# Kernel tuning notes

Hardware: AMD Instinct MI355X
Metric: run time of the kernel (lower is better)

Reference implementation:

```python
import jax, jax.numpy as jnp
import numpy as np

N_R = 20          # cfg['n_r']
H = 0.01          # cfg['h'] integration step
ALPHA_N = 0.1     # alpha(D_s_n, R_s_n) folded scale (stable: |eig(H*matAn)| << 2.8)
ALPHA_P = 0.08    # alpha(D_s_p, R_s_p)
BETA_N = -0.5     # -beta(...) for negative electrode
BETA_P = 0.4      # beta(...) for positive electrode


def _make_mats():
    n = N_R - 1
    # FDM tridiagonal (1,-2,1) radial diffusion stencil (spm_model.matA)
    matA = (jnp.diag(-2.0 * jnp.ones(n))
            + jnp.diag(jnp.ones(n - 1), 1)
            + jnp.diag(jnp.ones(n - 1), -1)).astype(jnp.float32)
    # boundary-flux input vector (spm_model.matB): only surface node driven
    matB = jnp.zeros(n, jnp.float32).at[-1].set(1.0)
    matAn = ALPHA_N * matA
    matBn = ALPHA_N * BETA_N * matB
    matAp = ALPHA_P * matA
    matBp = ALPHA_P * BETA_P * matB
    return matAn, matBn, matAp, matBp


def setup_inputs() -> dict:
    key = jax.random.key(0)
    k1, k2 = jax.random.split(key)
    n = N_R - 1
    B, K = 4096, 1024
    x = jax.random.normal(k1, (B, 2 * n), jnp.float32)
    i_seq = jax.random.normal(k2, (B, K), jnp.float32)
    matAn, matBn, matAp, matBp = _make_mats()
    return {"x": x, "i_seq": i_seq,
            "matAn": matAn, "matBn": matBn,
            "matAp": matAp, "matBp": matBp,
            "k": K}


def _rk4_step(x, i_col, A, Bv):
    # f(x) = A @ x + B * i  (batched: x [B,n], i_col [B,1], Bv [n])
    def f(y):
        return y @ A.T + i_col * Bv
    k1 = f(x)
    k2 = f(x + 0.5 * H * k1)
    k3 = f(x + 0.5 * H * k2)
    k4 = f(x + H * k3)
    return x + (H / 6.0) * (k1 + 2.0 * k2 + 2.0 * k3 + k4)


def reference(x, i_seq, matAn, matBn, matAp, matBp, k):
    n = N_R - 1
    xn0, xp0 = x[:, :n], x[:, n:]

    def step(carry, i_t):
        xn, xp = carry
        i_col = i_t[:, None]                      # [B,1]
        xn = _rk4_step(xn, i_col, matAn, matBn)
        xp = _rk4_step(xp, i_col, matAp, matBp)
        return (xn, xp), jnp.concatenate([xn, xp], axis=1)  # [B, 2n]

    _, x_all = jax.lax.scan(step, (xn0, xp0), i_seq.T)      # [k, B, 2n]
    return jnp.transpose(x_all, (1, 2, 0))                  # [B, 2n, k]
```

## Files before the change

kernel.cpp:

```cpp
#include <hip/hip_runtime.h>

#define NCOMP 19
#define NB    4096
#define PI_F  3.14159265358979323846f

typedef float f32x4 __attribute__((ext_vector_type(4)));

__device__ __forceinline__ constexpr float vconst(int k, int j) {
  constexpr float S[21] = {
    0.0f, 0.15643446504023087f, 0.3090169943749474f, 0.45399049973954675f,
    0.5877852522924731f, 0.7071067811865476f, 0.8090169943749475f,
    0.8910065241883679f, 0.9510565162951535f, 0.9876883405951378f, 1.0f,
    0.9876883405951378f, 0.9510565162951535f, 0.8910065241883679f,
    0.8090169943749475f, 0.7071067811865476f, 0.5877852522924731f,
    0.45399049973954675f, 0.3090169943749474f, 0.15643446504023087f, 0.0f};
  int m = ((k + 1) * (j + 1)) % 40;
  float s = (m <= 20) ? S[m] : -S[m - 20];
  return s * 0.31622776601683794f;
}

template <int CTRL, int RMASK>
__device__ __forceinline__ float dpp_add(float x) {
  int v = __builtin_amdgcn_update_dpp(0, __float_as_int(x), CTRL, RMASK, 0xf, true);
  return x + __int_as_float(v);
}
__device__ __forceinline__ float wave_iscan(float x) {
  x = dpp_add<0x111, 0xf>(x);
  x = dpp_add<0x112, 0xf>(x);
  x = dpp_add<0x114, 0xf>(x);
  x = dpp_add<0x118, 0xf>(x);
  x = dpp_add<0x142, 0xa>(x);
  x = dpp_add<0x143, 0xc>(x);
  return x;
}

__device__ __forceinline__ void derivf(const float* __restrict__ y, float a, float bin,
                                       float* __restrict__ k) {
#pragma unroll
  for (int j = 0; j < NCOMP; ++j) {
    float s = -2.0f * y[j];
    if (j > 0) s += y[j - 1];
    if (j < NCOMP - 1) s += y[j + 1];
    k[j] = a * s;
  }
  k[NCOMP - 1] += bin;
}

__device__ __forceinline__ void rk4f(float* __restrict__ x, float a, float bin) {
  const float h = 0.01f, h2 = 0.005f, h6 = 0.01f / 6.0f;
  float k[NCOMP], y[NCOMP], acc[NCOMP];
  derivf(x, a, bin, k);
#pragma unroll
  for (int j = 0; j < NCOMP; ++j) { acc[j] = k[j]; y[j] = fmaf(h2, k[j], x[j]); }
  derivf(y, a, bin, k);
#pragma unroll
  for (int j = 0; j < NCOMP; ++j) { acc[j] = fmaf(2.0f, k[j], acc[j]); y[j] = fmaf(h2, k[j], x[j]); }
  derivf(y, a, bin, k);
#pragma unroll
  for (int j = 0; j < NCOMP; ++j) { acc[j] = fmaf(2.0f, k[j], acc[j]); y[j] = fmaf(h, k[j], x[j]); }
  derivf(y, a, bin, k);
#pragma unroll
  for (int j = 0; j < NCOMP; ++j) x[j] = fmaf(h6, acc[j] + k[j], x[j]);
}

__device__ __forceinline__ void stage(float c, const float* __restrict__ u,
                                      const float* __restrict__ x,
                                      float* __restrict__ o) {
  o[0] = fmaf(c, fmaf(-2.0f, u[0], u[1]), x[0]);
#pragma unroll
  for (int j = 1; j < NCOMP - 1; ++j)
    o[j] = fmaf(c, fmaf(-2.0f, u[j], u[j - 1] + u[j + 1]), x[j]);
  o[NCOMP - 1] = fmaf(c, fmaf(-2.0f, u[NCOMP - 1], u[NCOMP - 2]), x[NCOMP - 1]);
}

__device__ __forceinline__ void step_horner(float* __restrict__ x, float ha,
                                            const float4 d, float iin) {
  float t1[NCOMP], t2[NCOMP];
  stage(ha * 0.25f, x, x, t1);
  stage(ha * (1.0f / 3.0f), t1, x, t2);
  stage(ha * 0.5f, t2, x, t1);
  stage(ha, t1, x, x);
  x[15] = fmaf(iin, d.x, x[15]);
  x[16] = fmaf(iin, d.y, x[16]);
  x[17] = fmaf(iin, d.z, x[17]);
  x[18] = fmaf(iin, d.w, x[18]);
}

__global__ __launch_bounds__(256) void spm_fused(
    const float* __restrict__ xin, const float* __restrict__ iseq,
    const float* __restrict__ An, const float* __restrict__ Bn,
    const float* __restrict__ Ap, const float* __restrict__ Bp,
    float* __restrict__ out)
{
  __shared__ float xs0[NCOMP];
  __shared__ float4 mcv[NCOMP];
  __shared__ __align__(16) float wtot[NCOMP][4];
  __shared__ float4 dls[2];

  const int t = threadIdx.x;
  const int lane = t & 63, wid = t >> 6;
  const int b = blockIdx.x >> 1, sys = blockIdx.x & 1;
  const float alpha = sys ? Ap[1] : An[1];
  const float ha    = 0.01f * alpha;

  if (t < 2) {
    float al  = t ? Ap[1] : An[1];
    float abv = t ? Bp[NCOMP - 1] : Bn[NCOMP - 1];
    float z[NCOMP];
#pragma unroll
    for (int j = 0; j < NCOMP; ++j) z[j] = 0.0f;
    rk4f(z, al, abv);
    dls[t] = make_float4(z[15], z[16], z[17], z[18]);
  }
  if (t < NCOMP) xs0[t] = xin[(size_t)b * (2 * NCOMP) + sys * NCOMP + t];
  __syncthreads();

  if (t < NCOMP) {
    float ab = sys ? Bp[NCOMP - 1] : Bn[NCOMP - 1];
    float sk = sinf((float)(t + 1) * (PI_F / 40.0f));
    float z  = ha * (-4.0f * sk * sk);
    float g  = 1.0f + z * (1.0f + z * (0.5f + z * ((1.0f/6.0f) + z * (1.0f/24.0f))));
    float S  = 1.0f + z * (0.5f + z * ((1.0f/6.0f) + z * (1.0f/24.0f)));
    float gi = 1.0f / g;
    float vlast = sinf((float)(((t + 1) * NCOMP) % 40) * (PI_F / 20.0f)) *
                  0.31622776601683794f;
    float s0 = 0.0f;
#pragma unroll
    for (int j = 0; j < NCOMP; ++j)
      s0 = fmaf(sinf((float)(((t + 1) * (j + 1)) % 40) * (PI_F / 20.0f)) *
                    0.31622776601683794f, xs0[j], s0);
    mcv[t] = make_float4(gi, 0.01f * S * ab * vlast * gi, __builtin_log2f(g), s0);
  }
  __syncthreads();

  const float4 dvec = dls[sys];
  const float4 iv = *reinterpret_cast<const float4*>(iseq + (size_t)b * 1024 + t * 4);
  const float pos = (float)(4 * t);

  float Cp[NCOMP];
#pragma unroll
  for (int k = 0; k < NCOMP; ++k) {
    const float4 c = mcv[k];
    float r = iv.x + c.x * (iv.y + c.x * (iv.z + c.x * iv.w));
    float a = __builtin_exp2f(-pos * c.z) * r;
    float v = wave_iscan(a);
    if (lane == 63) wtot[k][wid] = v;
    Cp[k] = v - a;
  }
  __syncthreads();

  float x0[NCOMP];
#pragma unroll
  for (int j = 0; j < NCOMP; ++j) x0[j] = 0.0f;
#pragma unroll
  for (int k = 0; k < NCOMP; ++k) {
    const float4 c = mcv[k];
    float4 q = *reinterpret_cast<const float4*>(&wtot[k][0]);
    float C = Cp[k];
    if (wid > 0) C += q.x;
    if (wid > 1) C += q.y;
    if (wid > 2) C += q.z;
    float s = __builtin_exp2f(pos * c.z) * fmaf(c.y, C, c.w);
#pragma unroll
    for (int j = 0; j < NCOMP; ++j) x0[j] = fmaf(s, vconst(k, j), x0[j]);
  }
  if (t == 0) {
#pragma unroll
    for (int j = 0; j < NCOMP; ++j) x0[j] = xs0[j];
  }

  float b0[NCOMP], b1[NCOMP], b2[NCOMP], b3[NCOMP];
  step_horner(x0, ha, dvec, iv.x);
#pragma unroll
  for (int j = 0; j < NCOMP; ++j) b0[j] = x0[j];
  step_horner(x0, ha, dvec, iv.y);
#pragma unroll
  for (int j = 0; j < NCOMP; ++j) b1[j] = x0[j];
  step_horner(x0, ha, dvec, iv.z);
#pragma unroll
  for (int j = 0; j < NCOMP; ++j) b2[j] = x0[j];
  step_horner(x0, ha, dvec, iv.w);
#pragma unroll
  for (int j = 0; j < NCOMP; ++j) b3[j] = x0[j];

  float* orow = out + ((size_t)b * (2 * NCOMP) + sys * NCOMP) * 1024 + t * 4;
#pragma unroll
  for (int j = 0; j < NCOMP; ++j) {
    f32x4 v = { b0[j], b1[j], b2[j], b3[j] };
    __builtin_nontemporal_store(v, reinterpret_cast<f32x4*>(orow + (size_t)j * 1024));
  }
}

extern "C" void kernel_launch(void* const* d_in, const int* in_sizes, int n_in,
                              void* d_out, int out_size, void* d_ws, size_t ws_size,
                              hipStream_t stream) {
  const float* x    = (const float*)d_in[0];
  const float* iseq = (const float*)d_in[1];
  const float* An   = (const float*)d_in[2];
  const float* Bn   = (const float*)d_in[3];
  const float* Ap   = (const float*)d_in[4];
  const float* Bp   = (const float*)d_in[5];
  float* out = (float*)d_out;

  spm_fused<<<NB * 2, 256, 0, stream>>>(x, iseq, An, Bn, Ap, Bp, out);
}
```

Measured before the change: 140.7 us.

## Advance four time steps in modal space and exploit sine-basis symmetry

The four per-thread RK4 steps now run in the diagonal eigen (sine) basis as scalar recurrences s←g·s+w·i, replacing the tridiagonal Horner stages in physical space. The modal-to-physical transform then uses even/odd mode symmetry (v[k][18-j] = ±v[k][j]) so each pair of output rows shares one set of partial sums. This also drops the per-block RK4 impulse precompute. Thread 0's exact initial-state override is gone, so its output now comes entirely from the modal reconstruction, which may change rounding slightly.

Measured after the change: 149.0 us. 1.06x slower.

```diff
diff --git a/kernel.cpp b/kernel.cpp
--- a/kernel.cpp
+++ b/kernel.cpp
@@ -34,58 +34,6 @@
   return x;
 }
 
-__device__ __forceinline__ void derivf(const float* __restrict__ y, float a, float bin,
-                                       float* __restrict__ k) {
-#pragma unroll
-  for (int j = 0; j < NCOMP; ++j) {
-    float s = -2.0f * y[j];
-    if (j > 0) s += y[j - 1];
-    if (j < NCOMP - 1) s += y[j + 1];
-    k[j] = a * s;
-  }
-  k[NCOMP - 1] += bin;
-}
-
-__device__ __forceinline__ void rk4f(float* __restrict__ x, float a, float bin) {
-  const float h = 0.01f, h2 = 0.005f, h6 = 0.01f / 6.0f;
-  float k[NCOMP], y[NCOMP], acc[NCOMP];
-  derivf(x, a, bin, k);
-#pragma unroll
-  for (int j = 0; j < NCOMP; ++j) { acc[j] = k[j]; y[j] = fmaf(h2, k[j], x[j]); }
-  derivf(y, a, bin, k);
-#pragma unroll
-  for (int j = 0; j < NCOMP; ++j) { acc[j] = fmaf(2.0f, k[j], acc[j]); y[j] = fmaf(h2, k[j], x[j]); }
-  derivf(y, a, bin, k);
-#pragma unroll
-  for (int j = 0; j < NCOMP; ++j) { acc[j] = fmaf(2.0f, k[j], acc[j]); y[j] = fmaf(h, k[j], x[j]); }
-  derivf(y, a, bin, k);
-#pragma unroll
-  for (int j = 0; j < NCOMP; ++j) x[j] = fmaf(h6, acc[j] + k[j], x[j]);
-}
-
-__device__ __forceinline__ void stage(float c, const float* __restrict__ u,
-                                      const float* __restrict__ x,
-                                      float* __restrict__ o) {
-  o[0] = fmaf(c, fmaf(-2.0f, u[0], u[1]), x[0]);
-#pragma unroll
-  for (int j = 1; j < NCOMP - 1; ++j)
-    o[j] = fmaf(c, fmaf(-2.0f, u[j], u[j - 1] + u[j + 1]), x[j]);
-  o[NCOMP - 1] = fmaf(c, fmaf(-2.0f, u[NCOMP - 1], u[NCOMP - 2]), x[NCOMP - 1]);
-}
-
-__device__ __forceinline__ void step_horner(float* __restrict__ x, float ha,
-                                            const float4 d, float iin) {
-  float t1[NCOMP], t2[NCOMP];
-  stage(ha * 0.25f, x, x, t1);
-  stage(ha * (1.0f / 3.0f), t1, x, t2);
-  stage(ha * 0.5f, t2, x, t1);
-  stage(ha, t1, x, x);
-  x[15] = fmaf(iin, d.x, x[15]);
-  x[16] = fmaf(iin, d.y, x[16]);
-  x[17] = fmaf(iin, d.z, x[17]);
-  x[18] = fmaf(iin, d.w, x[18]);
-}
-
 __global__ __launch_bounds__(256) void spm_fused(
     const float* __restrict__ xin, const float* __restrict__ iseq,
     const float* __restrict__ An, const float* __restrict__ Bn,
@@ -94,8 +42,8 @@
 {
   __shared__ float xs0[NCOMP];
   __shared__ float4 mcv[NCOMP];
+  __shared__ float2 mgw[NCOMP];
   __shared__ __align__(16) float wtot[NCOMP][4];
-  __shared__ float4 dls[2];
 
   const int t = threadIdx.x;
   const int lane = t & 63, wid = t >> 6;
@@ -103,15 +51,6 @@
   const float alpha = sys ? Ap[1] : An[1];
   const float ha    = 0.01f * alpha;
 
-  if (t < 2) {
-    float al  = t ? Ap[1] : An[1];
-    float abv = t ? Bp[NCOMP - 1] : Bn[NCOMP - 1];
-    float z[NCOMP];
-#pragma unroll
-    for (int j = 0; j < NCOMP; ++j) z[j] = 0.0f;
-    rk4f(z, al, abv);
-    dls[t] = make_float4(z[15], z[16], z[17], z[18]);
-  }
   if (t < NCOMP) xs0[t] = xin[(size_t)b * (2 * NCOMP) + sys * NCOMP + t];
   __syncthreads();
 
@@ -124,16 +63,17 @@
     float gi = 1.0f / g;
     float vlast = sinf((float)(((t + 1) * NCOMP) % 40) * (PI_F / 20.0f)) *
                   0.31622776601683794f;
+    float w = 0.01f * S * ab * vlast;
     float s0 = 0.0f;
 #pragma unroll
     for (int j = 0; j < NCOMP; ++j)
       s0 = fmaf(sinf((float)(((t + 1) * (j + 1)) % 40) * (PI_F / 20.0f)) *
                     0.31622776601683794f, xs0[j], s0);
-    mcv[t] = make_float4(gi, 0.01f * S * ab * vlast * gi, __builtin_log2f(g), s0);
+    mcv[t] = make_float4(gi, w * gi, __builtin_log2f(g), s0);
+    mgw[t] = make_float2(g, w);
   }
   __syncthreads();
 
-  const float4 dvec = dls[sys];
   const float4 iv = *reinterpret_cast<const float4*>(iseq + (size_t)b * 1024 + t * 4);
   const float pos = (float)(4 * t);
 
@@ -149,45 +89,55 @@
   }
   __syncthreads();
 
-  float x0[NCOMP];
-#pragma unroll
-  for (int j = 0; j < NCOMP; ++j) x0[j] = 0.0f;
+  float sA[NCOMP], sB[NCOMP], sC[NCOMP], sD[NCOMP];
 #pragma unroll
   for (int k = 0; k < NCOMP; ++k) {
     const float4 c = mcv[k];
+    const float2 gw = mgw[k];
     float4 q = *reinterpret_cast<const float4*>(&wtot[k][0]);
     float C = Cp[k];
     if (wid > 0) C += q.x;
     if (wid > 1) C += q.y;
     if (wid > 2) C += q.z;
     float s = __builtin_exp2f(pos * c.z) * fmaf(c.y, C, c.w);
-#pragma unroll
-    for (int j = 0; j < NCOMP; ++j) x0[j] = fmaf(s, vconst(k, j), x0[j]);
+    sA[k] = fmaf(gw.x, s,     gw.y * iv.x);
+    sB[k] = fmaf(gw.x, sA[k], gw.y * iv.y);
+    sC[k] = fmaf(gw.x, sB[k], gw.y * iv.z);
+    sD[k] = fmaf(gw.x, sC[k], gw.y * iv.w);
   }
-  if (t == 0) {
-#pragma unroll
-    for (int j = 0; j < NCOMP; ++j) x0[j] = xs0[j];
-  }
-
-  float b0[NCOMP], b1[NCOMP], b2[NCOMP], b3[NCOMP];
-  step_horner(x0, ha, dvec, iv.x);
-#pragma unroll
-  for (int j = 0; j < NCOMP; ++j) b0[j] = x0[j];
-  step_horner(x0, ha, dvec, iv.y);
-#pragma unroll
-  for (int j = 0; j < NCOMP; ++j) b1[j] = x0[j];
-  step_horner(x0, ha, dvec, iv.z);
-#pragma unroll
-  for (int j = 0; j < NCOMP; ++j) b2[j] = x0[j];
-  step_horner(x0, ha, dvec, iv.w);
-#pragma unroll
-  for (int j = 0; j < NCOMP; ++j) b3[j] = x0[j];
 
   float* orow = out + ((size_t)b * (2 * NCOMP) + sys * NCOMP) * 1024 + t * 4;
 #pragma unroll
-  for (int j = 0; j < NCOMP; ++j) {
-    f32x4 v = { b0[j], b1[j], b2[j], b3[j] };
-    __builtin_nontemporal_store(v, reinterpret_cast<f32x4*>(orow + (size_t)j * 1024));
+  for (int jj = 0; jj < 9; ++jj) {
+    float E0 = 0.f, E1 = 0.f, E2 = 0.f, E3 = 0.f;
+    float O0 = 0.f, O1 = 0.f, O2 = 0.f, O3 = 0.f;
+#pragma unroll
+    for (int k = 0; k < NCOMP; k += 2) {
+      const float vk = vconst(k, jj);
+      E0 = fmaf(sA[k], vk, E0); E1 = fmaf(sB[k], vk, E1);
+      E2 = fmaf(sC[k], vk, E2); E3 = fmaf(sD[k], vk, E3);
+    }
+#pragma unroll
+    for (int k = 1; k < NCOMP; k += 2) {
+      const float vk = vconst(k, jj);
+      O0 = fmaf(sA[k], vk, O0); O1 = fmaf(sB[k], vk, O1);
+      O2 = fmaf(sC[k], vk, O2); O3 = fmaf(sD[k], vk, O3);
+    }
+    f32x4 vp = { E0 + O0, E1 + O1, E2 + O2, E3 + O3 };
+    f32x4 vm = { E0 - O0, E1 - O1, E2 - O2, E3 - O3 };
+    __builtin_nontemporal_store(vp, reinterpret_cast<f32x4*>(orow + (size_t)jj * 1024));
+    __builtin_nontemporal_store(vm, reinterpret_cast<f32x4*>(orow + (size_t)(18 - jj) * 1024));
+  }
+  {
+    float E0 = 0.f, E1 = 0.f, E2 = 0.f, E3 = 0.f;
+#pragma unroll
+    for (int k = 0; k < NCOMP; k += 2) {
+      const float vk = vconst(k, 9);
+      E0 = fmaf(sA[k], vk, E0); E1 = fmaf(sB[k], vk, E1);
+      E2 = fmaf(sC[k], vk, E2); E3 = fmaf(sD[k], vk, E3);
+    }
+    f32x4 vc = { E0, E1, E2, E3 };
+    __builtin_nontemporal_store(vc, reinterpret_cast<f32x4*>(orow + (size_t)9 * 1024));
   }
 }
 
```
